# Performance work log

Measured on AMD Instinct MI355X. Metric: run time of the kernel, lower is better.

## Reference

```python
import jax, jax.numpy as jnp
import numpy as np

KNN = 11  # self.knn in VoronoiBaseNN


def setup_inputs() -> dict:
    key = jax.random.key(0)
    k1, k2 = jax.random.split(key)
    points = jax.random.normal(k1, (2, 50000, 3), dtype=jnp.float32)   # GT surface samples
    spoints = jax.random.normal(k2, (2, 4000, 3), dtype=jnp.float32)   # Voronoi generators
    return {"points": points, "spoints": spoints}


def reference(points, spoints):
    # Pairwise squared distances: [B, N, M]
    d2 = ((points[:, :, None, :] - spoints[:, None, :, :]) ** 2).sum(-1)
    # KNN smallest, sorted ascending (torch.topk(largest=False, sorted=True))
    _, idx = jax.lax.top_k(-d2, KNN)            # idx: [B, N, KNN]
    # Gather the KNN generator coordinates: [B, N, KNN, 3]
    gathered = jax.vmap(lambda sp, i: sp[i])(spoints, idx)
    inside = gathered[:, :, 0, :]               # closest cell center [B, N, 3]
    point_to_center = points - inside           # [B, N, 3]
    # Voronoi edge vectors to the other KNN-1 neighbors: [B, N, KNN-1, 3]
    voronoi_edge = gathered[:, :, 1:, :] - inside[:, :, None, :]
    edge_l = jnp.sqrt((voronoi_edge ** 2).sum(-1))                      # [B, N, KNN-1]
    vector_length = (point_to_center[:, :, None, :] * voronoi_edge).sum(-1) / edge_l
    sq_dist = (vector_length - edge_l / 2.0) ** 2
    return sq_dist.min(-1)                      # [B, N]
```

## Files before the change

### kernel.cpp

```cpp
#include <hip/hip_runtime.h>
#include <math.h>

#define NPTS  50000
#define NSP   4000
#define NGRP  1000
#define NW    4
#define QW    (NGRP / NW)
#define KNN   11
#define BIG   3.4e38f
#define SEGCAP 512
#define SEGPAD 8
#define SEGSTR (SEGCAP + SEGPAD)
#define GRIDC 32
#define NKEY  65536

#define MED3(a,b,c) __builtin_amdgcn_fmed3f((a),(b),(c))

__device__ unsigned g_hist[NKEY];
__device__ float4   g_sorted[2 * NPTS];

static __device__ __forceinline__ unsigned spread5(unsigned v) {
    return (v & 1u) | ((v & 2u) << 2) | ((v & 4u) << 4) |
           ((v & 8u) << 6) | ((v & 16u) << 8);
}

static __device__ __forceinline__ unsigned cell_key(int b, float x, float y, float z) {
    int gx = (int)floorf((x + 4.0f) * 4.0f);
    int gy = (int)floorf((y + 4.0f) * 4.0f);
    int gz = (int)floorf((z + 4.0f) * 4.0f);
    gx = min(max(gx, 0), GRIDC - 1);
    gy = min(max(gy, 0), GRIDC - 1);
    gz = min(max(gz, 0), GRIDC - 1);
    unsigned m = spread5((unsigned)gx) | (spread5((unsigned)gy) << 1) |
                 (spread5((unsigned)gz) << 2);
    return ((unsigned)b << 15) | m;
}

__global__ void k_zero() {
    int t = blockIdx.x * 256 + threadIdx.x;
    if (t < NKEY) g_hist[t] = 0u;
}

__global__ void k_hist(const float* __restrict__ pts) {
    int n = blockIdx.x * 256 + threadIdx.x;
    if (n >= 2 * NPTS) return;
    const float* p = pts + (size_t)n * 3;
    int b = (n >= NPTS) ? 1 : 0;
    atomicAdd(&g_hist[cell_key(b, p[0], p[1], p[2])], 1u);
}

__global__ void k_scan() {
    __shared__ unsigned part[1024];
    const int t = threadIdx.x;
    const unsigned base = (unsigned)blockIdx.x * 32768u + (unsigned)t * 32u;
    unsigned s = 0;
#pragma unroll
    for (int j = 0; j < 32; ++j) s += g_hist[base + j];
    part[t] = s;
    __syncthreads();
    for (int off = 1; off < 1024; off <<= 1) {
        unsigned v = (t >= off) ? part[t - off] : 0u;
        __syncthreads();
        part[t] += v;
        __syncthreads();
    }
    unsigned run = (unsigned)blockIdx.x * (unsigned)NPTS + part[t] - s;
#pragma unroll
    for (int j = 0; j < 32; ++j) {
        unsigned h = g_hist[base + j];
        g_hist[base + j] = run;
        run += h;
    }
}

__global__ void k_scatter(const float* __restrict__ pts) {
    int n = blockIdx.x * 256 + threadIdx.x;
    if (n >= 2 * NPTS) return;
    const float* p = pts + (size_t)n * 3;
    int b = (n >= NPTS) ? 1 : 0;
    float x = p[0], y = p[1], z = p[2];
    unsigned dst = atomicAdd(&g_hist[cell_key(b, x, y, z)], 1u);
    if (dst < 2u * NPTS)
        g_sorted[dst] = make_float4(x, y, z, __uint_as_float((unsigned)(n - b * NPTS)));
}

static __device__ __forceinline__ float wred_min(float v) {
#pragma unroll
    for (int off = 32; off > 0; off >>= 1) v = fminf(v, __shfl_xor(v, off, 64));
    return v;
}
static __device__ __forceinline__ float sred_min16(float v) {
#pragma unroll
    for (int off = 8; off > 0; off >>= 1) v = fminf(v, __shfl_xor(v, off, 64));
    return v;
}
static __device__ __forceinline__ float sred_max16(float v) {
#pragma unroll
    for (int off = 8; off > 0; off >>= 1) v = fmaxf(v, __shfl_xor(v, off, 64));
    return v;
}

__global__ __launch_bounds__(256, 3) void voronoi_kernel(
    const float* __restrict__ spts,
    float* __restrict__ out)
{
    __shared__ float4 sl[NW * SEGSTR];
    __shared__ float  lds_d[NW][64][13];
    __shared__ int    lds_i[NW][64];
    __shared__ float  lds_b[NW][64];
    __shared__ float  lds_m[NW][4];

    const int b    = blockIdx.y;
    const int lane = threadIdx.x & 63;
    const int wq   = threadIdx.x >> 6;
    int pi = blockIdx.x * 64 + lane;
    const bool valid = (pi < NPTS);
    if (!valid) pi = NPTS - 1;

    const float4 P = g_sorted[(size_t)b * NPTS + pi];
    const float px = P.x, py = P.y, pz = P.z;
    const unsigned orig = __float_as_uint(P.w);

    const float smnx = sred_min16(px), smxx = sred_max16(px);
    const float smny = sred_min16(py), smxy = sred_max16(py);
    const float smnz = sred_min16(pz), smxz = sred_max16(pz);
    const float scx = 0.5f * (smnx + smxx);
    const float scy = 0.5f * (smny + smxy);
    const float scz = 0.5f * (smnz + smxz);
    const float sR = sqrtf(sred_max16(
        fmaf(px - scx, px - scx, fmaf(py - scy, py - scy, (pz - scz) * (pz - scz)))));

#define BC(v, j) __shfl((v), (j) * 16, 64)
    const float b0nx = BC(smnx,0), b0xx = BC(smxx,0), b0ny = BC(smny,0),
                b0xy = BC(smxy,0), b0nz = BC(smnz,0), b0xz = BC(smxz,0),
                c0x = BC(scx,0), c0y = BC(scy,0), c0z = BC(scz,0), R0 = BC(sR,0);
    const float b1nx = BC(smnx,1), b1xx = BC(smxx,1), b1ny = BC(smny,1),
                b1xy = BC(smxy,1), b1nz = BC(smnz,1), b1xz = BC(smxz,1),
                c1x = BC(scx,1), c1y = BC(scy,1), c1z = BC(scz,1), R1 = BC(sR,1);
    const float b2nx = BC(smnx,2), b2xx = BC(smxx,2), b2ny = BC(smny,2),
                b2xy = BC(smxy,2), b2nz = BC(smnz,2), b2xz = BC(smxz,2),
                c2x = BC(scx,2), c2y = BC(scy,2), c2z = BC(scz,2), R2 = BC(sR,2);
    const float b3nx = BC(smnx,3), b3xx = BC(smxx,3), b3ny = BC(smny,3),
                b3xy = BC(smxy,3), b3nz = BC(smnz,3), b3xz = BC(smxz,3),
                c3x = BC(scx,3), c3y = BC(scy,3), c3z = BC(scz,3), R3 = BC(sR,3);

    const float4* __restrict__ spq = (const float4*)(spts + (size_t)b * NSP * 3);
    const int g0 = wq * QW, g1 = g0 + QW;

    float v0 = BIG, v1 = BIG, v2 = BIG, v3 = BIG;
    for (int k0 = g0; k0 < g1; k0 += 64) {
        const int g  = k0 + lane;
        const int gc = (g < g1) ? g : (g1 - 1);
        const float4 q0 = spq[3 * gc + 0];
        const float4 q1 = spq[3 * gc + 1];
        const float4 q2 = spq[3 * gc + 2];
        float t0 = BIG, t1 = BIG, t2 = BIG, t3 = BIG;
#define DACC(sx, sy, sz) { \
        float dx, dy, dz; \
        dx=(sx)-c0x; dy=(sy)-c0y; dz=(sz)-c0z; t0=fminf(t0, fmaf(dx,dx,fmaf(dy,dy,dz*dz))); \
        dx=(sx)-c1x; dy=(sy)-c1y; dz=(sz)-c1z; t1=fminf(t1, fmaf(dx,dx,fmaf(dy,dy,dz*dz))); \
        dx=(sx)-c2x; dy=(sy)-c2y; dz=(sz)-c2z; t2=fminf(t2, fmaf(dx,dx,fmaf(dy,dy,dz*dz))); \
        dx=(sx)-c3x; dy=(sy)-c3y; dz=(sz)-c3z; t3=fminf(t3, fmaf(dx,dx,fmaf(dy,dy,dz*dz))); }
        DACC(q0.x, q0.y, q0.z);
        DACC(q0.w, q1.x, q1.y);
        DACC(q1.z, q1.w, q2.x);
        DACC(q2.y, q2.z, q2.w);
        if (g < g1) { v0 = fminf(v0, t0); v1 = fminf(v1, t1);
                      v2 = fminf(v2, t2); v3 = fminf(v3, t3); }
    }

    float m0 = 0.f, m1 = 0.f, m2 = 0.f, m3 = 0.f;
#pragma unroll
    for (int t = 0; t < KNN; ++t) {
        m0 = wred_min(v0); v0 = (v0 == m0) ? BIG : v0;
        m1 = wred_min(v1); v1 = (v1 == m1) ? BIG : v1;
        m2 = wred_min(v2); v2 = (v2 == m2) ? BIG : v2;
        m3 = wred_min(v3); v3 = (v3 == m3) ? BIG : v3;
    }
    if (lane == 0) { lds_m[wq][0] = m0; lds_m[wq][1] = m1;
                     lds_m[wq][2] = m2; lds_m[wq][3] = m3; }
    __syncthreads();
    float M0 = BIG, M1 = BIG, M2 = BIG, M3 = BIG;
#pragma unroll
    for (int q = 0; q < NW; ++q) {
        M0 = fminf(M0, lds_m[q][0]); M1 = fminf(M1, lds_m[q][1]);
        M2 = fminf(M2, lds_m[q][2]); M3 = fminf(M3, lds_m[q][3]);
    }
    const float Tr0 = sqrtf(M0) + R0; const float T0 = Tr0*Tr0*1.0004f + 1e-12f;
    const float Tr1 = sqrtf(M1) + R1; const float T1 = Tr1*Tr1*1.0004f + 1e-12f;
    const float Tr2 = sqrtf(M2) + R2; const float T2 = Tr2*Tr2*1.0004f + 1e-12f;
    const float Tr3 = sqrtf(M3) + R3; const float T3 = Tr3*Tr3*1.0004f + 1e-12f;

#define BOXD2(sx,sy,sz, nx,xx,ny,xy,nz,xz) \
    (fmaf(MED3((sx),(nx),(xx))-(sx), MED3((sx),(nx),(xx))-(sx), \
     fmaf(MED3((sy),(ny),(xy))-(sy), MED3((sy),(ny),(xy))-(sy), \
          (MED3((sz),(nz),(xz))-(sz)) * (MED3((sz),(nz),(xz))-(sz)))))
#define ADM4(sx, sy, sz) \
    ((BOXD2(sx,sy,sz, b0nx,b0xx,b0ny,b0xy,b0nz,b0xz) <= T0) || \
     (BOXD2(sx,sy,sz, b1nx,b1xx,b1ny,b1xy,b1nz,b1xz) <= T1) || \
     (BOXD2(sx,sy,sz, b2nx,b2xx,b2ny,b2xy,b2nz,b2xz) <= T2) || \
     (BOXD2(sx,sy,sz, b3nx,b3xx,b3ny,b3xy,b3nz,b3xz) <= T3))

    const int segbase = wq * SEGSTR;
    unsigned cnt = 0;

    auto padseg = [&]() {
        if (lane < SEGPAD)
            sl[segbase + (int)cnt + lane] =
                make_float4(1e18f, 1e18f, 1e18f, __uint_as_float(0x7fffffffu));
    };

#define PUSH(sx, sy, sz, ok, idx) { \
        const unsigned long long msk = __ballot(ok); \
        if (ok) { \
            const unsigned pos = cnt + \
                __builtin_amdgcn_mbcnt_hi((unsigned)(msk >> 32), \
                    __builtin_amdgcn_mbcnt_lo((unsigned)msk, 0u)); \
            sl[segbase + (int)pos] = \
                make_float4((sx), (sy), (sz), __uint_as_float((unsigned)(idx))); \
        } \
        cnt += (unsigned)__popcll(msk); }

    auto run_pass = [&](auto&& consume) -> bool {
        bool of = false;
        cnt = 0;
        for (int k0 = g0; k0 < g1; k0 += 64) {
            if (cnt > (unsigned)(SEGCAP - 256)) {
                padseg(); consume(cnt); cnt = 0; of = true;
            }
            const int g  = k0 + lane;
            const int gc = (g < g1) ? g : (g1 - 1);
            const bool in = (g < g1);
            const float4 q0 = spq[3 * gc + 0];
            const float4 q1 = spq[3 * gc + 1];
            const float4 q2 = spq[3 * gc + 2];
            const bool a0 = in && ADM4(q0.x, q0.y, q0.z);
            const bool a1 = in && ADM4(q0.w, q1.x, q1.y);
            const bool a2 = in && ADM4(q1.z, q1.w, q2.x);
            const bool a3 = in && ADM4(q2.y, q2.z, q2.w);
            PUSH(q0.x, q0.y, q0.z, a0, 4 * gc + 0);
            PUSH(q0.w, q1.x, q1.y, a1, 4 * gc + 1);
            PUSH(q1.z, q1.w, q2.x, a2, 4 * gc + 2);
            PUSH(q2.y, q2.z, q2.w, a3, 4 * gc + 3);
        }
        padseg(); consume(cnt);
        return of;
    };

    float d0 = BIG, d1 = BIG, d2 = BIG, d3 = BIG, d4 = BIG, d5 = BIG,
          d6 = BIG, d7 = BIG, d8 = BIG, d9 = BIG, d10 = BIG;
    int i0 = 0x7fffffff;

#define CHAIN(nd, jj) { \
        if (__ballot((nd) < d10)) { \
            d10 = MED3(d9, d10, (nd)); \
            d9  = MED3(d8, d9,  (nd)); \
            d8  = MED3(d7, d8,  (nd)); \
            d7  = MED3(d6, d7,  (nd)); \
            d6  = MED3(d5, d6,  (nd)); \
            d5  = MED3(d4, d5,  (nd)); \
            d4  = MED3(d3, d4,  (nd)); \
            d3  = MED3(d2, d3,  (nd)); \
            d2  = MED3(d1, d2,  (nd)); \
            d1  = MED3(d0, d1,  (nd)); \
            i0  = ((nd) < d0) ? (jj) : i0; \
            d0  = fminf(d0, (nd)); \
        } }
#define CANDA(c) { \
        const float dx = px - (c).x, dy = py - (c).y, dz = pz - (c).z; \
        const float nd = fmaf(dx, dx, fmaf(dy, dy, dz * dz)); \
        const int jj = (int)__float_as_uint((c).w); \
        CHAIN(nd, jj); }

    auto chainA = [&](unsigned n) {
        if (n == 0u) return;
        float4 e0 = sl[segbase + 0], e1 = sl[segbase + 1],
               e2 = sl[segbase + 2], e3 = sl[segbase + 3];
        for (unsigned k = 0; k < n; k += 4) {
            const float4 n0 = sl[segbase + (int)k + 4];
            const float4 n1 = sl[segbase + (int)k + 5];
            const float4 n2 = sl[segbase + (int)k + 6];
            const float4 n3 = sl[segbase + (int)k + 7];
            CANDA(e0); CANDA(e1); CANDA(e2); CANDA(e3);
            e0 = n0; e1 = n1; e2 = n2; e3 = n3;
        }
    };

    const bool ovfA = run_pass(chainA);
    const unsigned cntA = cnt;

    lds_d[wq][lane][0]  = d0;  lds_d[wq][lane][1]  = d1;
    lds_d[wq][lane][2]  = d2;  lds_d[wq][lane][3]  = d3;
    lds_d[wq][lane][4]  = d4;  lds_d[wq][lane][5]  = d5;
    lds_d[wq][lane][6]  = d6;  lds_d[wq][lane][7]  = d7;
    lds_d[wq][lane][8]  = d8;  lds_d[wq][lane][9]  = d9;
    lds_d[wq][lane][10] = d10;
    lds_i[wq][lane] = i0;
    __syncthreads();

    float gb = BIG; int gi = 0x7fffffff;
#pragma unroll
    for (int q = 0; q < NW; ++q) {
        const float dq = lds_d[q][lane][0];
        const int   iq = lds_i[q][lane];
        const bool take = (dq < gb) || (dq == gb && iq < gi);
        gb = take ? dq : gb;
        gi = take ? iq : gi;
    }
#define INS(v) { \
        d10 = MED3(d9, d10, (v)); \
        d9  = MED3(d8, d9,  (v)); \
        d8  = MED3(d7, d8,  (v)); \
        d7  = MED3(d6, d7,  (v)); \
        d6  = MED3(d5, d6,  (v)); \
        d5  = MED3(d4, d5,  (v)); \
        d4  = MED3(d3, d4,  (v)); \
        d3  = MED3(d2, d3,  (v)); \
        d2  = MED3(d1, d2,  (v)); \
        d1  = MED3(d0, d1,  (v)); \
        d0  = fminf(d0, (v)); }
#pragma unroll
    for (int q = 0; q < NW; ++q) {
        if (q == wq) continue;
#pragma unroll
        for (int k = 0; k < 11; ++k) INS(lds_d[q][lane][k]);
    }
    const float d10g = d10;
    const int   i0g  = gi;

    const float* ip = spts + (size_t)b * NSP * 3 + (size_t)(unsigned)i0g * 3;
    const float ix = ip[0], iy = ip[1], iz = ip[2];
    const float vx = px - ix, vy = py - iy, vz = pz - iz;
    float best = BIG;

#define CANDB(c) { \
        const float dx = px - (c).x, dy = py - (c).y, dz = pz - (c).z; \
        const float nd = fmaf(dx, dx, fmaf(dy, dy, dz * dz)); \
        const int jj = (int)__float_as_uint((c).w); \
        const bool adm = (nd <= d10g) && (jj != i0g); \
        if (__ballot(adm)) { \
            const float ex = (c).x - ix, ey = (c).y - iy, ez = (c).z - iz; \
            const float ee = fmaf(ex, ex, fmaf(ey, ey, ez * ez)); \
            const float dt = fmaf(vx, ex, fmaf(vy, ey, vz * ez)); \
            const float u  = fmaf(-0.5f, ee, dt); \
            const float t2 = u * u * __builtin_amdgcn_rcpf(ee); \
            best = adm ? fminf(best, t2) : best; \
        } }

    auto scanB = [&](unsigned n) {
        if (n == 0u) return;
        float4 e0 = sl[segbase + 0], e1 = sl[segbase + 1],
               e2 = sl[segbase + 2], e3 = sl[segbase + 3];
        for (unsigned k = 0; k < n; k += 4) {
            const float4 n0 = sl[segbase + (int)k + 4];
            const float4 n1 = sl[segbase + (int)k + 5];
            const float4 n2 = sl[segbase + (int)k + 6];
            const float4 n3 = sl[segbase + (int)k + 7];
            CANDB(e0); CANDB(e1); CANDB(e2); CANDB(e3);
            e0 = n0; e1 = n1; e2 = n2; e3 = n3;
        }
    };

    if (!ovfA) {
        scanB(cntA);
    } else {
        (void)run_pass(scanB);
    }

    lds_b[wq][lane] = best;
    __syncthreads();
    if (wq == 0) {
        float m = fminf(fminf(lds_b[0][lane], lds_b[1][lane]),
                        fminf(lds_b[2][lane], lds_b[3][lane]));
        if (valid) out[(size_t)b * NPTS + orig] = m;
    }
}

extern "C" void kernel_launch(void* const* d_in, const int* in_sizes, int n_in,
                              void* d_out, int out_size, void* d_ws, size_t ws_size,
                              hipStream_t stream) {
    (void)in_sizes; (void)n_in; (void)d_ws; (void)ws_size; (void)out_size;
    const float* pts  = (const float*)d_in[0];
    const float* spts = (const float*)d_in[1];
    float* out = (float*)d_out;

    k_zero   <<<dim3(NKEY / 256),            dim3(256),  0, stream>>>();
    k_hist   <<<dim3((2 * NPTS + 255)/256),  dim3(256),  0, stream>>>(pts);
    k_scan   <<<dim3(2),                     dim3(1024), 0, stream>>>();
    k_scatter<<<dim3((2 * NPTS + 255)/256),  dim3(256),  0, stream>>>(pts);
    voronoi_kernel<<<dim3((NPTS + 63)/64, 2), dim3(256), 0, stream>>>(spts, out);
}
```

Before: 308.3 us.

## Split generator scan across 8 waves with single-box pruning and smaller segments

```diff
diff --git a/kernel.cpp b/kernel.cpp
--- a/kernel.cpp
+++ b/kernel.cpp
@@ -4,11 +4,11 @@
 #define NPTS  50000
 #define NSP   4000
 #define NGRP  1000
-#define NW    4
+#define NW    8
 #define QW    (NGRP / NW)
 #define KNN   11
 #define BIG   3.4e38f
-#define SEGCAP 512
+#define SEGCAP 128
 #define SEGPAD 8
 #define SEGSTR (SEGCAP + SEGPAD)
 #define GRIDC 32
@@ -89,18 +89,13 @@
     for (int off = 32; off > 0; off >>= 1) v = fminf(v, __shfl_xor(v, off, 64));
     return v;
 }
-static __device__ __forceinline__ float sred_min16(float v) {
-#pragma unroll
-    for (int off = 8; off > 0; off >>= 1) v = fminf(v, __shfl_xor(v, off, 64));
+static __device__ __forceinline__ float wred_max(float v) {
+#pragma unroll
+    for (int off = 32; off > 0; off >>= 1) v = fmaxf(v, __shfl_xor(v, off, 64));
     return v;
 }
-static __device__ __forceinline__ float sred_max16(float v) {
-#pragma unroll
-    for (int off = 8; off > 0; off >>= 1) v = fmaxf(v, __shfl_xor(v, off, 64));
-    return v;
-}
-
-__global__ __launch_bounds__(256, 3) void voronoi_kernel(
+
+__global__ __launch_bounds__(512, 6) void voronoi_kernel(
     const float* __restrict__ spts,
     float* __restrict__ out)
 {
@@ -108,7 +103,7 @@
     __shared__ float  lds_d[NW][64][13];
     __shared__ int    lds_i[NW][64];
     __shared__ float  lds_b[NW][64];
-    __shared__ float  lds_m[NW][4];
+    __shared__ float  lds_m[NW];
 
     const int b    = blockIdx.y;
     const int lane = threadIdx.x & 63;
@@ -121,85 +116,53 @@
     const float px = P.x, py = P.y, pz = P.z;
     const unsigned orig = __float_as_uint(P.w);
 
-    const float smnx = sred_min16(px), smxx = sred_max16(px);
-    const float smny = sred_min16(py), smxy = sred_max16(py);
-    const float smnz = sred_min16(pz), smxz = sred_max16(pz);
-    const float scx = 0.5f * (smnx + smxx);
-    const float scy = 0.5f * (smny + smxy);
-    const float scz = 0.5f * (smnz + smxz);
-    const float sR = sqrtf(sred_max16(
-        fmaf(px - scx, px - scx, fmaf(py - scy, py - scy, (pz - scz) * (pz - scz)))));
-
-#define BC(v, j) __shfl((v), (j) * 16, 64)
-    const float b0nx = BC(smnx,0), b0xx = BC(smxx,0), b0ny = BC(smny,0),
-                b0xy = BC(smxy,0), b0nz = BC(smnz,0), b0xz = BC(smxz,0),
-                c0x = BC(scx,0), c0y = BC(scy,0), c0z = BC(scz,0), R0 = BC(sR,0);
-    const float b1nx = BC(smnx,1), b1xx = BC(smxx,1), b1ny = BC(smny,1),
-                b1xy = BC(smxy,1), b1nz = BC(smnz,1), b1xz = BC(smxz,1),
-                c1x = BC(scx,1), c1y = BC(scy,1), c1z = BC(scz,1), R1 = BC(sR,1);
-    const float b2nx = BC(smnx,2), b2xx = BC(smxx,2), b2ny = BC(smny,2),
-                b2xy = BC(smxy,2), b2nz = BC(smnz,2), b2xz = BC(smxz,2),
-                c2x = BC(scx,2), c2y = BC(scy,2), c2z = BC(scz,2), R2 = BC(sR,2);
-    const float b3nx = BC(smnx,3), b3xx = BC(smxx,3), b3ny = BC(smny,3),
-                b3xy = BC(smxy,3), b3nz = BC(smnz,3), b3xz = BC(smxz,3),
-                c3x = BC(scx,3), c3y = BC(scy,3), c3z = BC(scz,3), R3 = BC(sR,3);
+    const float mnx = wred_min(px), mxx = wred_max(px);
+    const float mny = wred_min(py), mxy = wred_max(py);
+    const float mnz = wred_min(pz), mxz = wred_max(pz);
+    const float ccx = 0.5f * (mnx + mxx);
+    const float ccy = 0.5f * (mny + mxy);
+    const float ccz = 0.5f * (mnz + mxz);
+    const float R = sqrtf(wred_max(
+        fmaf(px - ccx, px - ccx, fmaf(py - ccy, py - ccy, (pz - ccz) * (pz - ccz)))));
 
     const float4* __restrict__ spq = (const float4*)(spts + (size_t)b * NSP * 3);
     const int g0 = wq * QW, g1 = g0 + QW;
 
-    float v0 = BIG, v1 = BIG, v2 = BIG, v3 = BIG;
+    float myMin = BIG;
     for (int k0 = g0; k0 < g1; k0 += 64) {
         const int g  = k0 + lane;
         const int gc = (g < g1) ? g : (g1 - 1);
         const float4 q0 = spq[3 * gc + 0];
         const float4 q1 = spq[3 * gc + 1];
         const float4 q2 = spq[3 * gc + 2];
-        float t0 = BIG, t1 = BIG, t2 = BIG, t3 = BIG;
-#define DACC(sx, sy, sz) { \
-        float dx, dy, dz; \
-        dx=(sx)-c0x; dy=(sy)-c0y; dz=(sz)-c0z; t0=fminf(t0, fmaf(dx,dx,fmaf(dy,dy,dz*dz))); \
-        dx=(sx)-c1x; dy=(sy)-c1y; dz=(sz)-c1z; t1=fminf(t1, fmaf(dx,dx,fmaf(dy,dy,dz*dz))); \
-        dx=(sx)-c2x; dy=(sy)-c2y; dz=(sz)-c2z; t2=fminf(t2, fmaf(dx,dx,fmaf(dy,dy,dz*dz))); \
-        dx=(sx)-c3x; dy=(sy)-c3y; dz=(sz)-c3z; t3=fminf(t3, fmaf(dx,dx,fmaf(dy,dy,dz*dz))); }
-        DACC(q0.x, q0.y, q0.z);
-        DACC(q0.w, q1.x, q1.y);
-        DACC(q1.z, q1.w, q2.x);
-        DACC(q2.y, q2.z, q2.w);
-        if (g < g1) { v0 = fminf(v0, t0); v1 = fminf(v1, t1);
-                      v2 = fminf(v2, t2); v3 = fminf(v3, t3); }
-    }
-
-    float m0 = 0.f, m1 = 0.f, m2 = 0.f, m3 = 0.f;
+        float dx = q0.x - ccx, dy = q0.y - ccy, dz = q0.z - ccz;
+        float md = fmaf(dx, dx, fmaf(dy, dy, dz * dz));
+        dx = q0.w - ccx; dy = q1.x - ccy; dz = q1.y - ccz;
+        md = fminf(md, fmaf(dx, dx, fmaf(dy, dy, dz * dz)));
+        dx = q1.z - ccx; dy = q1.w - ccy; dz = q2.x - ccz;
+        md = fminf(md, fmaf(dx, dx, fmaf(dy, dy, dz * dz)));
+        dx = q2.y - ccx; dy = q2.z - ccy; dz = q2.w - ccz;
+        md = fminf(md, fmaf(dx, dx, fmaf(dy, dy, dz * dz)));
+        if (g < g1) myMin = fminf(myMin, md);
+    }
+    float vv = myMin, m11 = 0.0f;
 #pragma unroll
     for (int t = 0; t < KNN; ++t) {
-        m0 = wred_min(v0); v0 = (v0 == m0) ? BIG : v0;
-        m1 = wred_min(v1); v1 = (v1 == m1) ? BIG : v1;
-        m2 = wred_min(v2); v2 = (v2 == m2) ? BIG : v2;
-        m3 = wred_min(v3); v3 = (v3 == m3) ? BIG : v3;
-    }
-    if (lane == 0) { lds_m[wq][0] = m0; lds_m[wq][1] = m1;
-                     lds_m[wq][2] = m2; lds_m[wq][3] = m3; }
+        m11 = wred_min(vv);
+        vv = (vv == m11) ? BIG : vv;
+    }
+    if (lane == 0) lds_m[wq] = m11;
     __syncthreads();
-    float M0 = BIG, M1 = BIG, M2 = BIG, M3 = BIG;
-#pragma unroll
-    for (int q = 0; q < NW; ++q) {
-        M0 = fminf(M0, lds_m[q][0]); M1 = fminf(M1, lds_m[q][1]);
-        M2 = fminf(M2, lds_m[q][2]); M3 = fminf(M3, lds_m[q][3]);
-    }
-    const float Tr0 = sqrtf(M0) + R0; const float T0 = Tr0*Tr0*1.0004f + 1e-12f;
-    const float Tr1 = sqrtf(M1) + R1; const float T1 = Tr1*Tr1*1.0004f + 1e-12f;
-    const float Tr2 = sqrtf(M2) + R2; const float T2 = Tr2*Tr2*1.0004f + 1e-12f;
-    const float Tr3 = sqrtf(M3) + R3; const float T3 = Tr3*Tr3*1.0004f + 1e-12f;
-
-#define BOXD2(sx,sy,sz, nx,xx,ny,xy,nz,xz) \
-    (fmaf(MED3((sx),(nx),(xx))-(sx), MED3((sx),(nx),(xx))-(sx), \
-     fmaf(MED3((sy),(ny),(xy))-(sy), MED3((sy),(ny),(xy))-(sy), \
-          (MED3((sz),(nz),(xz))-(sz)) * (MED3((sz),(nz),(xz))-(sz)))))
-#define ADM4(sx, sy, sz) \
-    ((BOXD2(sx,sy,sz, b0nx,b0xx,b0ny,b0xy,b0nz,b0xz) <= T0) || \
-     (BOXD2(sx,sy,sz, b1nx,b1xx,b1ny,b1xy,b1nz,b1xz) <= T1) || \
-     (BOXD2(sx,sy,sz, b2nx,b2xx,b2ny,b2xy,b2nz,b2xz) <= T2) || \
-     (BOXD2(sx,sy,sz, b3nx,b3xx,b3ny,b3xy,b3nz,b3xz) <= T3))
+    float m11g = BIG;
+#pragma unroll
+    for (int q = 0; q < NW; ++q) m11g = fminf(m11g, lds_m[q]);
+    const float Trad = sqrtf(m11g) + R;
+    const float T = Trad * Trad * 1.0004f + 1e-12f;
+
+#define ADM(sx, sy, sz) \
+    (fmaf(MED3((sx), mnx, mxx) - (sx), MED3((sx), mnx, mxx) - (sx), \
+     fmaf(MED3((sy), mny, mxy) - (sy), MED3((sy), mny, mxy) - (sy), \
+          (MED3((sz), mnz, mxz) - (sz)) * (MED3((sz), mnz, mxz) - (sz)))) <= T)
 
     const int segbase = wq * SEGSTR;
     unsigned cnt = 0;
@@ -210,7 +173,10 @@
                 make_float4(1e18f, 1e18f, 1e18f, __uint_as_float(0x7fffffffu));
     };
 
-#define PUSH(sx, sy, sz, ok, idx) { \
+#define PUSH(sx, sy, sz, ok, idx, CONSUME) { \
+        if (cnt > (unsigned)(SEGCAP - 64)) {                 \
+            padseg(); CONSUME(cnt); cnt = 0; of = true; \
+        } \
         const unsigned long long msk = __ballot(ok); \
         if (ok) { \
             const unsigned pos = cnt + \
@@ -221,31 +187,25 @@
         } \
         cnt += (unsigned)__popcll(msk); }
 
-    auto run_pass = [&](auto&& consume) -> bool {
-        bool of = false;
-        cnt = 0;
-        for (int k0 = g0; k0 < g1; k0 += 64) {
-            if (cnt > (unsigned)(SEGCAP - 256)) {
-                padseg(); consume(cnt); cnt = 0; of = true;
-            }
-            const int g  = k0 + lane;
-            const int gc = (g < g1) ? g : (g1 - 1);
-            const bool in = (g < g1);
-            const float4 q0 = spq[3 * gc + 0];
-            const float4 q1 = spq[3 * gc + 1];
-            const float4 q2 = spq[3 * gc + 2];
-            const bool a0 = in && ADM4(q0.x, q0.y, q0.z);
-            const bool a1 = in && ADM4(q0.w, q1.x, q1.y);
-            const bool a2 = in && ADM4(q1.z, q1.w, q2.x);
-            const bool a3 = in && ADM4(q2.y, q2.z, q2.w);
-            PUSH(q0.x, q0.y, q0.z, a0, 4 * gc + 0);
-            PUSH(q0.w, q1.x, q1.y, a1, 4 * gc + 1);
-            PUSH(q1.z, q1.w, q2.x, a2, 4 * gc + 2);
-            PUSH(q2.y, q2.z, q2.w, a3, 4 * gc + 3);
-        }
-        padseg(); consume(cnt);
-        return of;
-    };
+#define RUN_BUILD(CONSUME, ofvar) { \
+        ofvar = false; bool& of = ofvar; cnt = 0; \
+        for (int k0 = g0; k0 < g1; k0 += 64) { \
+            const int g  = k0 + lane; \
+            const int gc = (g < g1) ? g : (g1 - 1); \
+            const bool in = (g < g1); \
+            const float4 q0 = spq[3 * gc + 0]; \
+            const float4 q1 = spq[3 * gc + 1]; \
+            const float4 q2 = spq[3 * gc + 2]; \
+            const bool a0 = in && ADM(q0.x, q0.y, q0.z); \
+            const bool a1 = in && ADM(q0.w, q1.x, q1.y); \
+            const bool a2 = in && ADM(q1.z, q1.w, q2.x); \
+            const bool a3 = in && ADM(q2.y, q2.z, q2.w); \
+            PUSH(q0.x, q0.y, q0.z, a0, 4 * gc + 0, CONSUME); \
+            PUSH(q0.w, q1.x, q1.y, a1, 4 * gc + 1, CONSUME); \
+            PUSH(q1.z, q1.w, q2.x, a2, 4 * gc + 2, CONSUME); \
+            PUSH(q2.y, q2.z, q2.w, a3, 4 * gc + 3, CONSUME); \
+        } \
+        padseg(); CONSUME(cnt); }
 
     float d0 = BIG, d1 = BIG, d2 = BIG, d3 = BIG, d4 = BIG, d5 = BIG,
           d6 = BIG, d7 = BIG, d8 = BIG, d9 = BIG, d10 = BIG;
@@ -286,7 +246,8 @@
         }
     };
 
-    const bool ovfA = run_pass(chainA);
+    bool ovfA;
+    RUN_BUILD(chainA, ovfA);
     const unsigned cntA = cnt;
 
     lds_d[wq][lane][0]  = d0;  lds_d[wq][lane][1]  = d1;
@@ -323,7 +284,11 @@
     for (int q = 0; q < NW; ++q) {
         if (q == wq) continue;
 #pragma unroll
-        for (int k = 0; k < 11; ++k) INS(lds_d[q][lane][k]);
+        for (int k = 0; k < 11; ++k) {
+            const float v = lds_d[q][lane][k];
+            if (!__ballot(v < d10)) break;
+            INS(v);
+        }
     }
     const float d10g = d10;
     const int   i0g  = gi;
@@ -364,14 +329,17 @@
     if (!ovfA) {
         scanB(cntA);
     } else {
-        (void)run_pass(scanB);
+        bool ovfB;
+        RUN_BUILD(scanB, ovfB);
+        (void)ovfB;
     }
 
     lds_b[wq][lane] = best;
     __syncthreads();
     if (wq == 0) {
-        float m = fminf(fminf(lds_b[0][lane], lds_b[1][lane]),
-                        fminf(lds_b[2][lane], lds_b[3][lane]));
+        float m = lds_b[0][lane];
+#pragma unroll
+        for (int q = 1; q < NW; ++q) m = fminf(m, lds_b[q][lane]);
         if (valid) out[(size_t)b * NPTS + orig] = m;
     }
 }
@@ -388,5 +356,5 @@
     k_hist   <<<dim3((2 * NPTS + 255)/256),  dim3(256),  0, stream>>>(pts);
     k_scan   <<<dim3(2),                     dim3(1024), 0, stream>>>();
     k_scatter<<<dim3((2 * NPTS + 255)/256),  dim3(256),  0, stream>>>(pts);
-    voronoi_kernel<<<dim3((NPTS + 63)/64, 2), dim3(256), 0, stream>>>(spts, out);
-}
+    voronoi_kernel<<<dim3((NPTS + 63)/64, 2), dim3(512), 0, stream>>>(spts, out);
+}
```

Measured after the change: 258.3 us. 16.2% less time.
